# Kernel optimization log

Hardware: AMD Instinct MI355X
Metric: run time of the kernel (lower is better)

The kernel has to match this reference:

```python
import jax, jax.numpy as jnp
import numpy as np

NPOINT = 1024
RADIUS = 0.4
NSAMPLE = 32
BN_EPS = 1e-3  # keras BatchNormalization default epsilon


def _fps(xyz, npoint):
    # xyz: [N,3] -> indices [npoint] via farthest point sampling (seed index 0)
    N = xyz.shape[0]

    def step(carry, _):
        dists, far = carry
        d = jnp.sum((xyz - xyz[far]) ** 2, axis=-1)
        dists = jnp.minimum(dists, d)
        return (dists, jnp.argmax(dists).astype(jnp.int32)), far

    init = (jnp.full((N,), 1e10, dtype=xyz.dtype), jnp.asarray(0, dtype=jnp.int32))
    _, idx = jax.lax.scan(step, init, None, length=npoint)
    return idx


def _ball_query(xyz, new_xyz, radius, nsample):
    # xyz: [N,3], new_xyz: [S,3] -> idx [S,nsample]
    # First up-to-nsample points (in original index order) within radius of each
    # center; slots past the count are filled with the first found index
    # (matching the CUDA query_ball_point semantics).
    N = xyz.shape[0]
    d2 = jnp.sum((new_xyz[:, None, :] - xyz[None, :, :]) ** 2, axis=-1)  # [S,N]
    key = jnp.where(d2 < radius * radius, jnp.arange(N, dtype=jnp.int32), N)
    sk = jnp.sort(key, axis=-1)[:, :nsample]          # first valid indices, padded with N
    first = sk[:, :1]
    first = jnp.where(first < N, first, 0)            # fallback if no neighbor found
    idx = jnp.where(sk < N, sk, first)
    return idx.astype(jnp.int32)


def _gather(pts, idx):
    # pts: [B,N,C], idx: [B,...] -> [B,...,C]
    return jax.vmap(lambda p, i: p[i])(pts, idx)


def _conv_bn_relu(x, W, b, g, be):
    # 1x1 conv over [B,P,S,Cin] + batchnorm (training mode, batch stats) + relu
    y = jnp.einsum('bpsc,co->bpso', x, W) + b
    m = jnp.mean(y, axis=(0, 1, 2))
    v = jnp.var(y, axis=(0, 1, 2))
    y = (y - m) * jax.lax.rsqrt(v + BN_EPS) * g + be
    return jax.nn.relu(y)


def setup_inputs() -> dict:
    key = jax.random.key(0)
    ks = jax.random.split(key, 8)
    B, N, C = 16, 4096, 64
    xyz = jax.random.normal(ks[0], (B, N, 3), dtype=jnp.float32)
    points = jax.random.normal(ks[1], (B, N, C), dtype=jnp.float32)
    chans = [3 + C, 64, 64, 128]
    inp = {'xyz': xyz, 'points': points}
    for i in range(3):
        cin, cout = chans[i], chans[i + 1]
        limit = np.sqrt(6.0 / (cin + cout))  # glorot uniform
        inp[f'W{i}'] = jax.random.uniform(ks[2 + i], (cin, cout), jnp.float32, -limit, limit)
        inp[f'b{i}'] = jnp.zeros((cout,), jnp.float32)
        inp[f'g{i}'] = jnp.ones((cout,), jnp.float32)
        inp[f'be{i}'] = jnp.zeros((cout,), jnp.float32)
    return inp


def reference(xyz, points, W0, b0, g0, be0, W1, b1, g1, be1, W2, b2, g2, be2):
    xyz_c = jax.lax.stop_gradient(xyz)
    fps_idx = jax.vmap(lambda p: _fps(p, NPOINT))(xyz_c)           # [B,NPOINT]
    new_xyz = _gather(xyz, fps_idx)                                 # [B,NPOINT,3]
    idx = jax.vmap(lambda p, c: _ball_query(p, c, RADIUS, NSAMPLE))(
        xyz_c, jax.lax.stop_gradient(new_xyz))                      # [B,NPOINT,NSAMPLE]
    grouped_xyz = _gather(xyz, idx) - new_xyz[:, :, None, :]        # centered local coords
    grouped_points = _gather(points, idx)                           # [B,NPOINT,NSAMPLE,C]
    new_points = jnp.concatenate([grouped_xyz, grouped_points], axis=-1)
    new_points = _conv_bn_relu(new_points, W0, b0, g0, be0)
    new_points = _conv_bn_relu(new_points, W1, b1, g1, be1)
    new_points = _conv_bn_relu(new_points, W2, b2, g2, be2)
    new_points = jnp.max(new_points, axis=2)                        # max-pool over nsample
    return (new_xyz, new_points, idx)
```

## Files before the change

### kernel.cpp

```cpp
#include <hip/hip_runtime.h>

static constexpr int NB      = 16;
static constexpr int NPTS    = 4096;
static constexpr int NPOINTS = 1024;
static constexpr int NSAMP   = 32;
static constexpr int CIN0    = 67;
static constexpr int C0      = 64;
static constexpr int C1      = 64;
static constexpr int C2      = 128;
static constexpr size_t MROWS = (size_t)NB * NPOINTS * NSAMP;
#define RAD2 0.16f
#define BN_EPS 0.001f

__device__ __forceinline__ float4 uld4(const float* __restrict__ p) {
    return *(const float4* __restrict__)p;
}

__device__ __forceinline__ unsigned short f2bf(float f) {
    const unsigned u = __float_as_uint(f);
    return (unsigned short)((u + 0x7fffu + ((u >> 16) & 1u)) >> 16);
}
__device__ __forceinline__ float bf2f(unsigned short h) {
    return __uint_as_float((unsigned)h << 16);
}
// ... 112 lines not shown

    float px[8], py[8], pz[8], dd[8];
#pragma unroll
    for (int j = 0; j < 8; ++j) {
        const int i = tid + j * 512;
        px[j] = sx[i]; py[j] = sy[i]; pz[j] = sz[i];
        dd[j] = 1e10f;
    }

    int   far = 0;
    float fx = sx[0], fy = sy[0], fz = sz[0];
#pragma unroll 1
    for (int it = 0; it < NPOINTS; ++it) {
        if (tid == 0) sidx[it] = far;
        float bv = -1.0f; int bi = 0;
#pragma unroll
        for (int j = 0; j < 8; ++j) {
            const float dx = __fsub_rn(px[j], fx);
            const float dy = __fsub_rn(py[j], fy);
            const float dz = __fsub_rn(pz[j], fz);
            const float d  = __fadd_rn(__fadd_rn(__fmul_rn(dx, dx), __fmul_rn(dy, dy)),
                                       __fmul_rn(dz, dz));
            dd[j] = fminf(dd[j], d);
            if (dd[j] > bv) { bv = dd[j]; bi = tid + j * 512; }
        }
        unsigned long long k = ((unsigned long long)__float_as_uint(bv) << 32)
                             | (unsigned)(4095 - bi);
        kstep<0x111>(k);
        kstep<0x112>(k);
        kstep<0x114>(k);
        kstep<0x118>(k);
        kstep<0x142>(k);
        kstep<0x143>(k);

        const int pb = it & 1;
        if (lane == 63) redk[pb][wv] = k;
        __syncthreads();
        unsigned long long ck = redk[pb][0];
#pragma unroll
        for (int w = 1; w < 8; ++w) {
            const unsigned long long ok = redk[pb][w];
            if (ok > ck) ck = ok;
        }
        const int ci = 4095 - (int)(unsigned)(ck & 0xffffffffull);
        far = ci;
        fx = sx[ci]; fy = sy[ci]; fz = sz[ci];
    }
    __syncthreads();
    for (int it = tid; it < NPOINTS; it += 512) {
        const int ii = sidx[it];
        float* o = out_newxyz + ((size_t)b * NPOINTS + it) * 3;
        o[0] = sx[ii]; o[1] = sy[ii]; o[2] = sz[ii];
    }
}

__global__ __launch_bounds__(256) void ball_kernel(const float* __restrict__ xyz,
                                                   const float* __restrict__ newxyz,
                                                   float* __restrict__ out_idx_f)
{
    __shared__ int sel[4][NSAMP];
    const int tid  = threadIdx.x;
    const int lane = tid & 63;
    const int widx = tid >> 6;
    const int w = blockIdx.x * 4 + widx;
    const int b = w >> 10;

    const float cx = newxyz[(size_t)w * 3 + 0];
    const float cy = newxyz[(size_t)w * 3 + 1];
    const float cz = newxyz[(size_t)w * 3 + 2];
    const float* base = xyz + (size_t)b * NPTS * 3;

    int total = 0;
    for (int c = 0; c < NPTS / 64 && total < NSAMP; ++c) {
        const int n = c * 64 + lane;
        const float dx = __fsub_rn(cx, base[n * 3 + 0]);
        const float dy = __fsub_rn(cy, base[n * 3 + 1]);
        const float dz = __fsub_rn(cz, base[n * 3 + 2]);
        const float d2 = __fadd_rn(__fadd_rn(__fmul_rn(dx, dx), __fmul_rn(dy, dy)),
                                   __fmul_rn(dz, dz));
        const bool pred = d2 < RAD2;
        const unsigned long long mask = __ballot(pred);
        if (pred) {
            const int pos = total + (int)__popcll(mask & ((1ull << lane) - 1ull));
            if (pos < NSAMP) sel[widx][pos] = n;
        }
        total += (int)__popcll(mask);
    }
    __syncthreads();
    if (lane < NSAMP) {
        const int first = sel[widx][0];
        const int v = (lane < total) ? sel[widx][lane] : first;
        out_idx_f[(size_t)w * NSAMP + lane] = (float)v;
    }
}

__device__ __forceinline__ void stats4q(float a0, float a1, float a2, float a3,
                                        float* sa, bool wr)
{
    float q0 = a0*a0, q1 = a1*a1, q2 = a2*a2, q3 = a3*a3;
    a0 = dpp_psum16(a0); q0 = dpp_psum16(q0);
    a1 = dpp_psum16(a1); q1 = dpp_psum16(q1);
    a2 = dpp_psum16(a2); q2 = dpp_psum16(q2);
    a3 = dpp_psum16(a3); q3 = dpp_psum16(q3);
    if (wr) {
        sa[0] += a0; sa[1] += q0; sa[2] += a1; sa[3] += q1;
        sa[4] += a2; sa[5] += q2; sa[6] += a3; sa[7] += q3;
    }
}

__device__ __forceinline__ void stats4(float a0, float a1, float a2, float a3,
                                       float* sa, int lane)
{
    float q0 = a0*a0, q1 = a1*a1, q2 = a2*a2, q3 = a3*a3;
    a0 = dpp_sum64(a0); q0 = dpp_sum64(q0);
    a1 = dpp_sum64(a1); q1 = dpp_sum64(q1);
    a2 = dpp_sum64(a2); q2 = dpp_sum64(q2);
    a3 = dpp_sum64(a3); q3 = dpp_sum64(q3);
    if (lane == 63) {
        sa[0] += a0; sa[1] += q0; sa[2] += a1; sa[3] += q1;
        sa[4] += a2; sa[5] += q2; sa[6] += a3; sa[7] += q3;
    }
}

__device__ __forceinline__ void layer0_dedup(
    const float* __restrict__ xyz, const float* __restrict__ P,
    const float* __restrict__ newxyz, const float* __restrict__ idxf,
    const float* __restrict__ W0, const float* __restrict__ b0,
    int r, float* x1)
{
    const int i  = (int)idxf[r];
    const int bb = r >> 15;
    const int pp = (r >> 5) & 1023;
    const float* pz = xyz + ((size_t)bb * NPTS + i) * 3;
    const float* nz = newxyz + ((size_t)bb * NPOINTS + pp) * 3;
    const float r0 = pz[0] - nz[0];
    const float r1 = pz[1] - nz[1];
    const float r2 = pz[2] - nz[2];
    const float4* prow = (const float4*)(P + ((size_t)bb * NPTS + i) * 64);
#pragma unroll
    for (int oc = 0; oc < 16; ++oc) {
        const float4 pv = prow[oc];
        const float4 bv = uld4(b0 + 4 * oc);
        const float4 wa = uld4(W0 + 0 * 64 + 4 * oc);
        const float4 wb = uld4(W0 + 1 * 64 + 4 * oc);
        const float4 wc = uld4(W0 + 2 * 64 + 4 * oc);
        x1[4*oc+0] = fmaf(r0, wa.x, fmaf(r1, wb.x, fmaf(r2, wc.x, bv.x + pv.x)));
        x1[4*oc+1] = fmaf(r0, wa.y, fmaf(r1, wb.y, fmaf(r2, wc.y, bv.y + pv.y)));
        x1[4*oc+2] = fmaf(r0, wa.z, fmaf(r1, wb.z, fmaf(r2, wc.z, bv.z + pv.z)));
        x1[4*oc+3] = fmaf(r0, wa.w, fmaf(r1, wb.w, fmaf(r2, wc.w, bv.w + pv.w)));
    }
}

__global__ __launch_bounds__(256, 4) void pass0_kernel(
    const float* __restrict__ xyz, const float* __restrict__ P,
    const float* __restrict__ newxyz, const float* __restrict__ idxf,
    const float* __restrict__ W0, const float* __restrict__ b0,
    float* __restrict__ gstats)
{
    __shared__ float sacc[16][2 * C0];
    const int tid  = threadIdx.x;
    const int lane = tid & 63;
    const int wv   = tid >> 6;
    const int slot = wv * 4 + (lane >> 4);
    const bool wr  = (lane & 15) == 15;

    for (int j = tid; j < 16 * 2 * C0; j += 256) (&sacc[0][0])[j] = 0.f;
    __syncthreads();

    const int r = blockIdx.x * 256 + tid;
    float x1[C0];
    layer0_dedup(xyz, P, newxyz, idxf, W0, b0, r, x1);

#pragma unroll
    for (int oc = 0; oc < 16; ++oc)
        stats4q(x1[4*oc+0], x1[4*oc+1], x1[4*oc+2], x1[4*oc+3], &sacc[slot][8*oc], wr);

    __syncthreads();
    for (int j = tid; j < 2 * C0; j += 256) {
        float s = 0.f;
#pragma unroll
        for (int q = 0; q < 16; ++q) s += sacc[q][j];
        atomicAdd(&gstats[j], s);
    }
}

__global__ __launch_bounds__(256, 3) void pass1Y_kernel(
    const float* __restrict__ xyz, const float* __restrict__ P,
    const float* __restrict__ newxyz, const float* __restrict__ idxf,
    const float* __restrict__ W0, const float* __restrict__ b0,
    const float* __restrict__ W1, const float* __restrict__ b1,
    const float* __restrict__ ss0,
    float* __restrict__ gstats, unsigned short* __restrict__ y1b)
{
    __shared__ float sacc[16][2 * C0];
    const int tid  = threadIdx.x;
    const int lane = tid & 63;
    const int wv   = tid >> 6;
    const int slot = wv * 4 + (lane >> 4);
    const bool wr  = (lane & 15) == 15;

    for (int j = tid; j < 16 * 2 * C0; j += 256) (&sacc[0][0])[j] = 0.f;
    __syncthreads();

    const int r = blockIdx.x * 256 + tid;
    float x1[C0];
    layer0_dedup(xyz, P, newxyz, idxf, W0, b0, r, x1);
#pragma unroll
    for (int o = 0; o < C0; ++o)
        x1[o] = fmaxf(0.f, fmaf(x1[o], ss0[o], ss0[64 + o]));

    float y1[C1];
#pragma unroll
    for (int o = 0; o < C1; o += 4) {
        const float4 bv = uld4(b1 + o);
        y1[o] = bv.x; y1[o+1] = bv.y; y1[o+2] = bv.z; y1[o+3] = bv.w;
    }
#pragma unroll 2
    for (int k = 0; k < C0; ++k) {
        const float xk = x1[k];
#pragma unroll
        for (int oc = 0; oc < 16; ++oc) {
            const float4 w4 = uld4(W1 + k * 64 + 4 * oc);
            y1[4*oc+0] = fmaf(xk, w4.x, y1[4*oc+0]);
            y1[4*oc+1] = fmaf(xk, w4.y, y1[4*oc+1]);
            y1[4*oc+2] = fmaf(xk, w4.z, y1[4*oc+2]);
            y1[4*oc+3] = fmaf(xk, w4.w, y1[4*oc+3]);
        }
    }

#pragma unroll
    for (int oc = 0; oc < 16; ++oc)
        stats4q(y1[4*oc+0], y1[4*oc+1], y1[4*oc+2], y1[4*oc+3], &sacc[slot][8*oc], wr);

    uint4* yo = (uint4*)(y1b + (size_t)r * 64);
#pragma unroll
    for (int gq = 0; gq < 8; ++gq) {
        union { unsigned short u[8]; uint4 v; } pk;
#pragma unroll
        for (int e = 0; e < 8; ++e) pk.u[e] = f2bf(y1[8*gq+e]);
        yo[gq] = pk.v;
    }

    __syncthreads();
    for (int j = tid; j < 2 * C0; j += 256) {
        float s = 0.f;
#pragma unroll
        for (int q = 0; q < 16; ++q) s += sacc[q][j];
        atomicAdd(&gstats[j], s);
    }
}

__global__ __launch_bounds__(256, 3) void p2Ym_kernel(
    const unsigned short* __restrict__ y1b,
    const unsigned short* __restrict__ W2t,
    const float* __restrict__ b2,
    const float* __restrict__ ss1,
    float* __restrict__ gstats, float2* __restrict__ mnmx)
{
    __shared__ float  ssl[2 * C1];
    __shared__ float2 sacc[8][C2];
    __shared__ float2 mnacc[8][C2];

    const int tid  = threadIdx.x;
    const int lane = tid & 63;
    const int w    = tid >> 6;
    const int half = lane >> 5;
    const int col  = lane & 31;
    const int slot = w * 2 + half;

    for (int j = tid; j < 2 * C1; j += 256) ssl[j] = ss1[j];
    __syncthreads();

    const int r = blockIdx.x * 128 + w * 32 + col;

    UB afrag[4];
#pragma unroll
    for (int t = 0; t < 4; ++t) {
        const int ko = t * 16 + half * 8;
        uint4 ua = *(const uint4*)(y1b + (size_t)r * 64 + ko);
        float scs[8], shs[8];
        *(float4*)&scs[0] = *(const float4*)&ssl[ko];
        *(float4*)&scs[4] = *(const float4*)&ssl[ko + 4];
        *(float4*)&shs[0] = *(const float4*)&ssl[64 + ko];
        *(float4*)&shs[4] = *(const float4*)&ssl[64 + ko + 4];
        const unsigned* ud = (const unsigned*)&ua;
        uint4 outw;
        unsigned* od = (unsigned*)&outw;
#pragma unroll
        for (int d = 0; d < 4; ++d) {
            const float flo = bf2f((unsigned short)(ud[d] & 0xffffu));
            const float fhi = bf2f((unsigned short)(ud[d] >> 16));
            const float vlo = fmaxf(0.f, fmaf(flo, scs[2*d],   shs[2*d]));
            const float vhi = fmaxf(0.f, fmaf(fhi, scs[2*d+1], shs[2*d+1]));
            od[d] = ((unsigned)f2bf(vhi) << 16) | (unsigned)f2bf(vlo);
        }
        afrag[t].u = outw;
    }

#pragma unroll
    for (int ct = 0; ct < 4; ++ct) {
        const float bias = b2[ct * 32 + col];
        f32x16 acc;
#pragma unroll
        for (int i = 0; i < 16; ++i) acc[i] = bias;
#pragma unroll
        for (int t = 0; t < 4; ++t) {
            UB bfrag;
            bfrag.u = *(const uint4*)(W2t + (size_t)(ct * 32 + col) * 64 + t * 16 + half * 8);
            acc = __builtin_amdgcn_mfma_f32_32x32x16_bf16(afrag[t].h, bfrag.h, acc, 0, 0, 0);
        }
        float s = 0.f, q = 0.f, mn = 3.4e38f, mx = -3.4e38f;
#pragma unroll
        for (int i = 0; i < 16; ++i) {
            const float v = acc[i];
            s += v; q = fmaf(v, v, q);
            mn = fminf(mn, v); mx = fmaxf(mx, v);
        }
        sacc[slot][ct * 32 + col]  = make_float2(s, q);
        mnacc[slot][ct * 32 + col] = make_float2(mn, mx);
    }

    __syncthreads();
    for (int j = tid; j < C2; j += 256) {
        float s = 0.f, q = 0.f;
#pragma unroll
        for (int v = 0; v < 8; ++v) { s += sacc[v][j].x; q += sacc[v][j].y; }
        atomicAdd(&gstats[2*j], s);
        atomicAdd(&gstats[2*j+1], q);
    }
    for (int j = tid; j < 4 * C2; j += 256) {
        const int wg = j >> 7, ch = j & 127;
        const float2 a = mnacc[2*wg][ch], bq = mnacc[2*wg+1][ch];
        mnmx[((size_t)blockIdx.x * 4 + wg) * C2 + ch] =
            make_float2(fminf(a.x, bq.x), fmaxf(a.y, bq.y));
    }
}

__global__ __launch_bounds__(256) void finY_kernel(const float2* __restrict__ mnmx,
                                                   const float* __restrict__ gs2,
                                                   const float* __restrict__ g2,
                                                   const float* __restrict__ be2,
                                                   float* __restrict__ out_np)
{
    const int t = blockIdx.x * 256 + threadIdx.x;
    const int g = t >> 7;
    const int o = t & 127;
    const float inv  = 1.0f / (float)MROWS;
    const float mean = gs2[2*o] * inv;
    const float var  = fmaxf(0.f, gs2[2*o+1] * inv - mean * mean);
    const float sc   = g2[o] / sqrtf(var + BN_EPS);
    const float sh   = fmaf(-mean, sc, be2[o]);
    const float2 mm  = mnmx[(size_t)g * C2 + o];
    const float y    = (sc >= 0.f) ? mm.y : mm.x;
    out_np[t] = fmaxf(0.f, fmaf(y, sc, sh));
}

template<int C>
__global__ void ss_kernel(const float* __restrict__ gs, const float* __restrict__ g,
                          const float* __restrict__ be, float* __restrict__ ss)
{
    const int o = threadIdx.x;
    const float inv  = 1.0f / (float)MROWS;
    const float mean = gs[2*o] * inv;
    const float var  = fmaxf(0.f, gs[2*o+1] * inv - mean * mean);
    const float sc   = g[o] / sqrtf(var + BN_EPS);
    ss[o]     = sc;
    ss[C + o] = fmaf(-mean, sc, be[o]);
}

__global__ __launch_bounds__(256) void preP_kernel(const float* __restrict__ points,
                                                   const float* __restrict__ W0,
                                                   float* __restrict__ P)
{
    const int r = blockIdx.x * 256 + threadIdx.x;
    const float4* pr = (const float4*)(points + (size_t)r * 64);
    float x[64];
#pragma unroll
    for (int j = 0; j < 16; ++j) {
        const float4 v = pr[j];
        x[4*j+0] = v.x; x[4*j+1] = v.y; x[4*j+2] = v.z; x[4*j+3] = v.w;
    }
    float acc[64];
#pragma unroll
    for (int o = 0; o < 64; ++o) acc[o] = 0.f;
#pragma unroll 2
    for (int k = 0; k < 64; ++k) {
        const float xk = x[k];
#pragma unroll
        for (int oc = 0; oc < 16; ++oc) {
            const float4 w4 = uld4(W0 + (3 + k) * 64 + 4 * oc);
            acc[4*oc+0] = fmaf(xk, w4.x, acc[4*oc+0]);
            acc[4*oc+1] = fmaf(xk, w4.y, acc[4*oc+1]);
            acc[4*oc+2] = fmaf(xk, w4.z, acc[4*oc+2]);
            acc[4*oc+3] = fmaf(xk, w4.w, acc[4*oc+3]);
        }
    }
    float4* po = (float4*)(P + (size_t)r * 64);
#pragma unroll
    for (int oc = 0; oc < 16; ++oc)
        po[oc] = make_float4(acc[4*oc+0], acc[4*oc+1], acc[4*oc+2], acc[4*oc+3]);
}

template<int PHASE>
__global__ __launch_bounds__(256, 2) void passP_kernel(
    const float* __restrict__ xyz, const float* __restrict__ P,
    const float* __restrict__ newxyz, const float* __restrict__ idxf,
    const float* __restrict__ W0, const float* __restrict__ b0,
    const float* __restrict__ W1, const float* __restrict__ b1,
    const float* __restrict__ W2, const float* __restrict__ b2,
    const float* __restrict__ ss0, const float* __restrict__ ss1,
    const float* __restrict__ ss2,
    float* __restrict__ gstats, float* __restrict__ out_np)
{
    constexpr int CS = (PHASE == 2) ? C2 : C0;
    __shared__ float sacc[4][2 * CS];

    const int tid  = threadIdx.x;
    const int lane = tid & 63;
    const int wv   = tid >> 6;

    if constexpr (PHASE <= 2) {
        for (int j = tid; j < 8 * CS; j += 256) (&sacc[0][0])[j] = 0.f;
        __syncthreads();
    }

    const int r = blockIdx.x * 256 + tid;
    float x1[C0];
    layer0_dedup(xyz, P, newxyz, idxf, W0, b0, r, x1);

    if constexpr (PHASE == 0) {
#pragma unroll
        for (int oc = 0; oc < 16; ++oc)
            stats4(x1[4*oc+0], x1[4*oc+1], x1[4*oc+2], x1[4*oc+3], &sacc[wv][8*oc], lane);
    } else {
#pragma unroll
        for (int o = 0; o < C0; ++o)
            x1[o] = fmaxf(0.f, fmaf(x1[o], ss0[o], ss0[64 + o]));

        float y1[C1];
#pragma unroll
        for (int o = 0; o < C1; o += 4) {
            const float4 bv = uld4(b1 + o);
            y1[o] = bv.x; y1[o+1] = bv.y; y1[o+2] = bv.z; y1[o+3] = bv.w;
        }
#pragma unroll 2
        for (int k = 0; k < C0; ++k) {
            const float xk = x1[k];
#pragma unroll
            for (int oc = 0; oc < 16; ++oc) {
                const float4 w4 = uld4(W1 + k * 64 + 4 * oc);
                y1[4*oc+0] = fmaf(xk, w4.x, y1[4*oc+0]);
                y1[4*oc+1] = fmaf(xk, w4.y, y1[4*oc+1]);
                y1[4*oc+2] = fmaf(xk, w4.z, y1[4*oc+2]);
// ... 3 lines not shown

        if constexpr (PHASE == 1) {
#pragma unroll
            for (int oc = 0; oc < 16; ++oc)
                stats4(y1[4*oc+0], y1[4*oc+1], y1[4*oc+2], y1[4*oc+3], &sacc[wv][8*oc], lane);
        } else {
#pragma unroll
            for (int o = 0; o < C1; ++o)
                y1[o] = fmaxf(0.f, fmaf(y1[o], ss1[o], ss1[64 + o]));

            float a2[C2];
#pragma unroll
            for (int o = 0; o < C2; o += 4) {
                const float4 bv = uld4(b2 + o);
                a2[o] = bv.x; a2[o+1] = bv.y; a2[o+2] = bv.z; a2[o+3] = bv.w;
            }
#pragma unroll 2
            for (int k = 0; k < C1; ++k) {
                const float xk = y1[k];
#pragma unroll
                for (int o = 0; o < C2; o += 4) {
                    const float4 w4 = uld4(W2 + k * C2 + o);
                    a2[o+0] = fmaf(xk, w4.x, a2[o+0]);
                    a2[o+1] = fmaf(xk, w4.y, a2[o+1]);
                    a2[o+2] = fmaf(xk, w4.z, a2[o+2]);
                    a2[o+3] = fmaf(xk, w4.w, a2[o+3]);
                }
            }

            if constexpr (PHASE == 2) {
#pragma unroll
                for (int o = 0; o < C2; ++o) {
                    const float s = dpp_sum64(a2[o]);
                    const float q = dpp_sum64(a2[o] * a2[o]);
                    if (lane == 63) { sacc[wv][2*o] += s; sacc[wv][2*o+1] += q; }
                }
            } else {
                const int g = r >> 5;
#pragma unroll
                for (int o = 0; o < C2; ++o) {
                    float v = fmaxf(0.f, fmaf(a2[o], ss2[o], ss2[C2 + o]));
                    v = dpp_max32(v);
                    if (lane == 31 || lane == 63) out_np[(size_t)g * C2 + o] = v;
                }
            }
        }
    }

    if constexpr (PHASE <= 2) {
        __syncthreads();
        for (int j = tid; j < 2 * CS; j += 256)
            atomicAdd(&gstats[j], sacc[0][j] + sacc[1][j] + sacc[2][j] + sacc[3][j]);
    }
}

template<int PHASE>
__global__ __launch_bounds__(128) void pass_kernel(
    const float* __restrict__ xyz, const float* __restrict__ points,
    const float* __restrict__ newxyz, const float* __restrict__ idxf,
    const float* __restrict__ W0, const float* __restrict__ b0,
    const float* __restrict__ W1, const float* __restrict__ b1,
    const float* __restrict__ W2, const float* __restrict__ b2,
    const float* __restrict__ ss0, const float* __restrict__ ss1,
    const float* __restrict__ ss2,
    float* __restrict__ gstats, float* __restrict__ out_np)
{
    constexpr int CS = (PHASE == 2) ? C2 : C0;
    __shared__ float xld[(PHASE >= 1) ? (64 * 128) : 1];
    __shared__ float sacc[2][2 * CS];

    const int tid  = threadIdx.x;
    const int lane = tid & 63;
    const int wv   = tid >> 6;

    if constexpr (PHASE <= 2) {
        for (int j = tid; j < 2 * 2 * CS; j += 128) (&sacc[0][0])[j] = 0.f;
        __syncthreads();
    }

    const int r  = blockIdx.x * 128 + tid;
    const int i  = (int)idxf[r];
    const int bb = r >> 15;
    const int pp = (r >> 5) & 1023;

    float x[CIN0];
    {
        const float* pz = xyz + ((size_t)bb * NPTS + i) * 3;
        const float* nz = newxyz + ((size_t)bb * NPOINTS + pp) * 3;
        x[0] = pz[0] - nz[0];
        x[1] = pz[1] - nz[1];
        x[2] = pz[2] - nz[2];
        const float4* p4 = (const float4*)(points + ((size_t)bb * NPTS + i) * 64);
#pragma unroll
        for (int j = 0; j < 16; ++j) {
            const float4 v = p4[j];
            x[3+4*j+0] = v.x; x[3+4*j+1] = v.y; x[3+4*j+2] = v.z; x[3+4*j+3] = v.w;
        }
    }

#pragma unroll 1
    for (int oc = 0; oc < 16; ++oc) {
        const float4 bv = uld4(b0 + 4*oc);
        float a0 = bv.x, a1 = bv.y, a2 = bv.z, a3 = bv.w;
#pragma unroll
        for (int k = 0; k < CIN0; ++k) {
            const float4 w4 = uld4(W0 + k*64 + 4*oc);
// ... 83 lines not shown
        __syncthreads();
        for (int j = tid; j < 2 * CS; j += 128)
            atomicAdd(&gstats[j], sacc[0][j] + sacc[1][j]);
    }
}

extern "C" void kernel_launch(void* const* d_in, const int* in_sizes, int n_in,
                              void* d_out, int out_size, void* d_ws, size_t ws_size,
                              hipStream_t stream)
{
    (void)in_sizes; (void)n_in; (void)out_size;
    const float* xyz    = (const float*)d_in[0];
    const float* points = (const float*)d_in[1];
    const float* W0  = (const float*)d_in[2];
    const float* b0  = (const float*)d_in[3];
    const float* g0  = (const float*)d_in[4];
    const float* be0 = (const float*)d_in[5];
    const float* W1  = (const float*)d_in[6];
    const float* b1  = (const float*)d_in[7];
    const float* g1  = (const float*)d_in[8];
    const float* be1 = (const float*)d_in[9];
    const float* W2  = (const float*)d_in[10];
    const float* b2  = (const float*)d_in[11];
    const float* g2  = (const float*)d_in[12];
    const float* be2 = (const float*)d_in[13];

    float* out = (float*)d_out;
    float* out_newxyz = out;
    float* out_newpts = out + (size_t)NB * NPOINTS * 3;
    float* out_idx    = out_newpts + (size_t)NB * NPOINTS * C2;

    float* wsf = (float*)d_ws;
    float* gs0 = wsf + 0;
    float* gs1 = wsf + 128;
    float* gs2 = wsf + 256;
    float* ss0 = wsf + 512;
    float* ss1 = wsf + 640;
    float* ss2 = wsf + 768;
    const size_t PBYTES  = (size_t)NB * NPTS * C0 * 4;
    const size_t MMBYTES = (size_t)NB * NPOINTS * 2 * C2 * 4;
    const size_t YBYTES  = MROWS * C1 * 2;
    const size_t TBYTES  = (size_t)C2 * C1 * 2;
    float* P    = (float*)((char*)d_ws + 65536);
    float* mnmx = (float*)((char*)d_ws + 65536 + PBYTES);
    unsigned short* y1b = (unsigned short*)((char*)d_ws + 65536 + PBYTES + MMBYTES);
    unsigned short* W2t = (unsigned short*)((char*)d_ws + 65536 + PBYTES + MMBYTES + YBYTES);

    const bool haveP = ws_size >= (65536 + PBYTES);
    const bool haveY = ws_size >= (65536 + PBYTES + MMBYTES + YBYTES + TBYTES);

    const int frontGrid = NB + 1 + (haveP ? (NB * NPTS / 512) : 0);
    fps_kernel<<<frontGrid, 512, 0, stream>>>(xyz, out_newxyz, wsf, points, W0, P,
                                              W2, haveY ? W2t : nullptr);
    ball_kernel<<<(NB * NPOINTS) / 4, 256, 0, stream>>>(xyz, out_newxyz, out_idx);

    if (haveY) {
        const int grid = (int)(MROWS / 256);
        pass0_kernel<<<grid, 256, 0, stream>>>(xyz, P, out_newxyz, out_idx,
                                               W0, b0, gs0);
        ss_kernel<C0><<<1, C0, 0, stream>>>(gs0, g0, be0, ss0);
        pass1Y_kernel<<<grid, 256, 0, stream>>>(xyz, P, out_newxyz, out_idx,
                                                W0, b0, W1, b1, ss0, gs1, y1b);
        ss_kernel<C1><<<1, C1, 0, stream>>>(gs1, g1, be1, ss1);
        p2Ym_kernel<<<(int)(MROWS / 128), 256, 0, stream>>>(y1b, W2t, b2, ss1,
                                                            gs2, (float2*)mnmx);
        finY_kernel<<<NB * NPOINTS * C2 / 256, 256, 0, stream>>>((const float2*)mnmx,
                                                                 gs2, g2, be2, out_newpts);
    } else if (haveP) {
        const int grid = (int)(MROWS / 256);
        passP_kernel<0><<<grid, 256, 0, stream>>>(xyz, P, out_newxyz, out_idx,
                                                  W0, b0, W1, b1, W2, b2,
                                                  ss0, ss1, ss2, gs0, nullptr);
        ss_kernel<C0><<<1, C0, 0, stream>>>(gs0, g0, be0, ss0);
        passP_kernel<1><<<grid, 256, 0, stream>>>(xyz, P, out_newxyz, out_idx,
                                                  W0, b0, W1, b1, W2, b2,
                                                  ss0, ss1, ss2, gs1, nullptr);
        ss_kernel<C1><<<1, C1, 0, stream>>>(gs1, g1, be1, ss1);
        passP_kernel<2><<<grid, 256, 0, stream>>>(xyz, P, out_newxyz, out_idx,
                                                  W0, b0, W1, b1, W2, b2,
                                                  ss0, ss1, ss2, gs2, nullptr);
        ss_kernel<C2><<<1, C2, 0, stream>>>(gs2, g2, be2, ss2);
        passP_kernel<3><<<grid, 256, 0, stream>>>(xyz, P, out_newxyz, out_idx,
                                                  W0, b0, W1, b1, W2, b2,
                                                  ss0, ss1, ss2, nullptr, out_newpts);
    } else {
        const int grid = (int)(MROWS / 128);
        pass_kernel<0><<<grid, 128, 0, stream>>>(xyz, points, out_newxyz, out_idx,
                                                 W0, b0, W1, b1, W2, b2,
                                                 ss0, ss1, ss2, gs0, nullptr);
        ss_kernel<C0><<<1, C0, 0, stream>>>(gs0, g0, be0, ss0);
        pass_kernel<1><<<grid, 128, 0, stream>>>(xyz, points, out_newxyz, out_idx,
                                                 W0, b0, W1, b1, W2, b2,
                                                 ss0, ss1, ss2, gs1, nullptr);
        ss_kernel<C1><<<1, C1, 0, stream>>>(gs1, g1, be1, ss1);
        pass_kernel<2><<<grid, 128, 0, stream>>>(xyz, points, out_newxyz, out_idx,
                                                 W0, b0, W1, b1, W2, b2,
                                                 ss0, ss1, ss2, gs2, nullptr);
        ss_kernel<C2><<<1, C2, 0, stream>>>(gs2, g2, be2, ss2);
        pass_kernel<3><<<grid, 128, 0, stream>>>(xyz, points, out_newxyz, out_idx,
                                                 W0, b0, W1, b1, W2, b2,
                                                 ss0, ss1, ss2, nullptr, out_newpts);
    }
}
```

Measured before the change: 1.202 ms.

## Fuse ball query into layer-0 stats pass and inline BN scale computation

```diff
diff --git a/kernel.cpp b/kernel.cpp
--- a/kernel.cpp
+++ b/kernel.cpp
@@ -188,6 +188,336 @@
         float* o = out_newxyz + ((size_t)b * NPOINTS + it) * 3;
         o[0] = sx[ii]; o[1] = sy[ii]; o[2] = sz[ii];
     }
+}
+
+__device__ __forceinline__ void stats4q(float a0, float a1, float a2, float a3,
+                                        float* sa, bool wr)
+{
+    float q0 = a0*a0, q1 = a1*a1, q2 = a2*a2, q3 = a3*a3;
+    a0 = dpp_psum16(a0); q0 = dpp_psum16(q0);
+    a1 = dpp_psum16(a1); q1 = dpp_psum16(q1);
+    a2 = dpp_psum16(a2); q2 = dpp_psum16(q2);
+    a3 = dpp_psum16(a3); q3 = dpp_psum16(q3);
+    if (wr) {
+        sa[0] += a0; sa[1] += q0; sa[2] += a1; sa[3] += q1;
+        sa[4] += a2; sa[5] += q2; sa[6] += a3; sa[7] += q3;
+    }
+}
+
+__device__ __forceinline__ void stats4(float a0, float a1, float a2, float a3,
+                                       float* sa, int lane)
+{
+    float q0 = a0*a0, q1 = a1*a1, q2 = a2*a2, q3 = a3*a3;
+    a0 = dpp_sum64(a0); q0 = dpp_sum64(q0);
+    a1 = dpp_sum64(a1); q1 = dpp_sum64(q1);
+    a2 = dpp_sum64(a2); q2 = dpp_sum64(q2);
+    a3 = dpp_sum64(a3); q3 = dpp_sum64(q3);
+    if (lane == 63) {
+        sa[0] += a0; sa[1] += q0; sa[2] += a1; sa[3] += q1;
+        sa[4] += a2; sa[5] += q2; sa[6] += a3; sa[7] += q3;
+    }
+}
+
+__device__ __forceinline__ void layer0_body(
+    const float* __restrict__ xyz, const float* __restrict__ P,
+    const float* __restrict__ newxyz,
+    const float* __restrict__ W0, const float* __restrict__ b0,
+    int i, int bb, int pp, float* x1)
+{
+    const float* pz = xyz + ((size_t)bb * NPTS + i) * 3;
+    const float* nz = newxyz + ((size_t)bb * NPOINTS + pp) * 3;
+    const float r0 = pz[0] - nz[0];
+    const float r1 = pz[1] - nz[1];
+    const float r2 = pz[2] - nz[2];
+    const float4* prow = (const float4*)(P + ((size_t)bb * NPTS + i) * 64);
+#pragma unroll
+    for (int oc = 0; oc < 16; ++oc) {
+        const float4 pv = prow[oc];
+        const float4 bv = uld4(b0 + 4 * oc);
+        const float4 wa = uld4(W0 + 0 * 64 + 4 * oc);
+        const float4 wb = uld4(W0 + 1 * 64 + 4 * oc);
+        const float4 wc = uld4(W0 + 2 * 64 + 4 * oc);
+        x1[4*oc+0] = fmaf(r0, wa.x, fmaf(r1, wb.x, fmaf(r2, wc.x, bv.x + pv.x)));
+        x1[4*oc+1] = fmaf(r0, wa.y, fmaf(r1, wb.y, fmaf(r2, wc.y, bv.y + pv.y)));
+        x1[4*oc+2] = fmaf(r0, wa.z, fmaf(r1, wb.z, fmaf(r2, wc.z, bv.z + pv.z)));
+        x1[4*oc+3] = fmaf(r0, wa.w, fmaf(r1, wb.w, fmaf(r2, wc.w, bv.w + pv.w)));
+    }
+}
+
+__device__ __forceinline__ void layer0_dedup(
+    const float* __restrict__ xyz, const float* __restrict__ P,
+    const float* __restrict__ newxyz, const float* __restrict__ idxf,
+    const float* __restrict__ W0, const float* __restrict__ b0,
+    int r, float* x1)
+{
+    const int i  = (int)idxf[r];
+    const int bb = r >> 15;
+    const int pp = (r >> 5) & 1023;
+    layer0_body(xyz, P, newxyz, W0, b0, i, bb, pp, x1);
+}
+
+template<int C>
+__device__ __forceinline__ void bn_inline(const float* __restrict__ gs,
+                                          const float* __restrict__ g,
+                                          const float* __restrict__ be,
+                                          float* ssl, int tid)
+{
+    if (tid < C) {
+        const float inv  = 1.0f / (float)MROWS;
+        const float mean = gs[2*tid] * inv;
+        const float var  = fmaxf(0.f, gs[2*tid+1] * inv - mean * mean);
+        const float sc   = g[tid] / sqrtf(var + BN_EPS);
+        ssl[tid]     = sc;
+        ssl[C + tid] = fmaf(-mean, sc, be[tid]);
+    }
+}
+
+__global__ __launch_bounds__(256, 4) void ballP0_kernel(
+    const float* __restrict__ xyz, const float* __restrict__ P,
+    const float* __restrict__ newxyz,
+    const float* __restrict__ W0, const float* __restrict__ b0,
+    float* __restrict__ gstats, float* __restrict__ out_idx_f)
+{
+    __shared__ int   sel[8][NSAMP];
+    __shared__ int   stotal[8];
+    __shared__ float sacc[16][2 * C0];
+
+    const int tid  = threadIdx.x;
+    const int lane = tid & 63;
+    const int wv   = tid >> 6;
+
+    for (int j = tid; j < 16 * 2 * C0; j += 256) (&sacc[0][0])[j] = 0.f;
+
+#pragma unroll 1
+    for (int cc = 0; cc < 2; ++cc) {
+        const int lc = wv * 2 + cc;
+        const int w  = blockIdx.x * 8 + lc;
+        const int b  = w >> 10;
+        const float cx = newxyz[(size_t)w * 3 + 0];
+        const float cy = newxyz[(size_t)w * 3 + 1];
+        const float cz = newxyz[(size_t)w * 3 + 2];
+        const float* base = xyz + (size_t)b * NPTS * 3;
+
+        int total = 0;
+        for (int c = 0; c < NPTS / 64 && total < NSAMP; ++c) {
+            const int n = c * 64 + lane;
+            const float dx = __fsub_rn(cx, base[n * 3 + 0]);
+            const float dy = __fsub_rn(cy, base[n * 3 + 1]);
+            const float dz = __fsub_rn(cz, base[n * 3 + 2]);
+            const float d2 = __fadd_rn(__fadd_rn(__fmul_rn(dx, dx), __fmul_rn(dy, dy)),
+                                       __fmul_rn(dz, dz));
+            const bool pred = d2 < RAD2;
+            const unsigned long long mask = __ballot(pred);
+            if (pred) {
+                const int pos = total + (int)__popcll(mask & ((1ull << lane) - 1ull));
+                if (pos < NSAMP) sel[lc][pos] = n;
+            }
+            total += (int)__popcll(mask);
+        }
+        if (lane == 0) stotal[lc] = (total < NSAMP) ? total : NSAMP;
+    }
+    __syncthreads();
+
+    const int r  = blockIdx.x * 256 + tid;
+    const int ci = tid >> 5;
+    const int s  = tid & 31;
+    const int tt = stotal[ci];
+    const int n  = (s < tt) ? sel[ci][s] : sel[ci][0];
+    out_idx_f[r] = (float)n;
+
+    const int bb = r >> 15;
+    const int pp = (r >> 5) & 1023;
+    float x1[C0];
+    layer0_body(xyz, P, newxyz, W0, b0, n, bb, pp, x1);
+
+    const int slot = wv * 4 + (lane >> 4);
+    const bool wr  = (lane & 15) == 15;
+#pragma unroll
+    for (int oc = 0; oc < 16; ++oc)
+        stats4q(x1[4*oc+0], x1[4*oc+1], x1[4*oc+2], x1[4*oc+3], &sacc[slot][8*oc], wr);
+
+    __syncthreads();
+    for (int j = tid; j < 2 * C0; j += 256) {
+        float ssum = 0.f;
+#pragma unroll
+        for (int q = 0; q < 16; ++q) ssum += sacc[q][j];
+        atomicAdd(&gstats[j], ssum);
+    }
+}
+
+__global__ __launch_bounds__(256, 3) void pass1Y_kernel(
+    const float* __restrict__ xyz, const float* __restrict__ P,
+    const float* __restrict__ newxyz, const float* __restrict__ idxf,
+    const float* __restrict__ W0, const float* __restrict__ b0,
+    const float* __restrict__ W1, const float* __restrict__ b1,
+    const float* __restrict__ gs0, const float* __restrict__ g0,
+    const float* __restrict__ be0,
+    float* __restrict__ gstats, unsigned short* __restrict__ y1b)
+{
+    __shared__ float sacc[16][2 * C0];
+    __shared__ float ssl[2 * C0];
+    const int tid  = threadIdx.x;
+    const int lane = tid & 63;
+    const int wv   = tid >> 6;
+    const int slot = wv * 4 + (lane >> 4);
+    const bool wr  = (lane & 15) == 15;
+
+    for (int j = tid; j < 16 * 2 * C0; j += 256) (&sacc[0][0])[j] = 0.f;
+    bn_inline<C0>(gs0, g0, be0, ssl, tid);
+    __syncthreads();
+
+    const int r = blockIdx.x * 256 + tid;
+    float x1[C0];
+    layer0_dedup(xyz, P, newxyz, idxf, W0, b0, r, x1);
+#pragma unroll
+    for (int o = 0; o < C0; ++o)
+        x1[o] = fmaxf(0.f, fmaf(x1[o], ssl[o], ssl[64 + o]));
+
+    float y1[C1];
+#pragma unroll
+    for (int o = 0; o < C1; o += 4) {
+        const float4 bv = uld4(b1 + o);
+        y1[o] = bv.x; y1[o+1] = bv.y; y1[o+2] = bv.z; y1[o+3] = bv.w;
+    }
+#pragma unroll 2
+    for (int k = 0; k < C0; ++k) {
+        const float xk = x1[k];
+#pragma unroll
+        for (int oc = 0; oc < 16; ++oc) {
+            const float4 w4 = uld4(W1 + k * 64 + 4 * oc);
+            y1[4*oc+0] = fmaf(xk, w4.x, y1[4*oc+0]);
+            y1[4*oc+1] = fmaf(xk, w4.y, y1[4*oc+1]);
+            y1[4*oc+2] = fmaf(xk, w4.z, y1[4*oc+2]);
+            y1[4*oc+3] = fmaf(xk, w4.w, y1[4*oc+3]);
+        }
+    }
+
+#pragma unroll
+    for (int oc = 0; oc < 16; ++oc)
+        stats4q(y1[4*oc+0], y1[4*oc+1], y1[4*oc+2], y1[4*oc+3], &sacc[slot][8*oc], wr);
+
+    uint4* yo = (uint4*)(y1b + (size_t)r * 64);
+#pragma unroll
+    for (int gq = 0; gq < 8; ++gq) {
+        union { unsigned short u[8]; uint4 v; } pk;
+#pragma unroll
+        for (int e = 0; e < 8; ++e) pk.u[e] = f2bf(y1[8*gq+e]);
+        yo[gq] = pk.v;
+    }
+
+    __syncthreads();
+    for (int j = tid; j < 2 * C0; j += 256) {
+        float s = 0.f;
+#pragma unroll
+        for (int q = 0; q < 16; ++q) s += sacc[q][j];
+        atomicAdd(&gstats[j], s);
+    }
+}
+
+__global__ __launch_bounds__(256, 3) void p2Ym_kernel(
+    const unsigned short* __restrict__ y1b,
+    const unsigned short* __restrict__ W2t,
+    const float* __restrict__ b2,
+    const float* __restrict__ gs1, const float* __restrict__ g1,
+    const float* __restrict__ be1,
+    float* __restrict__ gstats, float2* __restrict__ mnmx)
+{
+    __shared__ float  ssl[2 * C1];
+    __shared__ float2 sacc[8][C2];
+    __shared__ float2 mnacc[8][C2];
+
+    const int tid  = threadIdx.x;
+    const int lane = tid & 63;
+    const int w    = tid >> 6;
+    const int half = lane >> 5;
+    const int col  = lane & 31;
+    const int slot = w * 2 + half;
+
+    bn_inline<C1>(gs1, g1, be1, ssl, tid);
+    __syncthreads();
+
+    const int r = blockIdx.x * 128 + w * 32 + col;
+
+    UB afrag[4];
+#pragma unroll
+    for (int t = 0; t < 4; ++t) {
+        const int ko = t * 16 + half * 8;
+        uint4 ua = *(const uint4*)(y1b + (size_t)r * 64 + ko);
+        float scs[8], shs[8];
+        *(float4*)&scs[0] = *(const float4*)&ssl[ko];
+        *(float4*)&scs[4] = *(const float4*)&ssl[ko + 4];
+        *(float4*)&shs[0] = *(const float4*)&ssl[64 + ko];
+        *(float4*)&shs[4] = *(const float4*)&ssl[64 + ko + 4];
+        const unsigned* ud = (const unsigned*)&ua;
+        uint4 outw;
+        unsigned* od = (unsigned*)&outw;
+#pragma unroll
+        for (int d = 0; d < 4; ++d) {
+            const float flo = bf2f((unsigned short)(ud[d] & 0xffffu));
+            const float fhi = bf2f((unsigned short)(ud[d] >> 16));
+            const float vlo = fmaxf(0.f, fmaf(flo, scs[2*d],   shs[2*d]));
+            const float vhi = fmaxf(0.f, fmaf(fhi, scs[2*d+1], shs[2*d+1]));
+            od[d] = ((unsigned)f2bf(vhi) << 16) | (unsigned)f2bf(vlo);
+        }
+        afrag[t].u = outw;
+    }
+
+#pragma unroll
+    for (int ct = 0; ct < 4; ++ct) {
+        const float bias = b2[ct * 32 + col];
+        f32x16 acc;
+#pragma unroll
+        for (int i = 0; i < 16; ++i) acc[i] = bias;
+#pragma unroll
+        for (int t = 0; t < 4; ++t) {
+            UB bfrag;
+            bfrag.u = *(const uint4*)(W2t + (size_t)(ct * 32 + col) * 64 + t * 16 + half * 8);
+            acc = __builtin_amdgcn_mfma_f32_32x32x16_bf16(afrag[t].h, bfrag.h, acc, 0, 0, 0);
+        }
+        float s = 0.f, q = 0.f, mn = 3.4e38f, mx = -3.4e38f;
+#pragma unroll
+        for (int i = 0; i < 16; ++i) {
+            const float v = acc[i];
+            s += v; q = fmaf(v, v, q);
+            mn = fminf(mn, v); mx = fmaxf(mx, v);
+        }
+        sacc[slot][ct * 32 + col]  = make_float2(s, q);
+        mnacc[slot][ct * 32 + col] = make_float2(mn, mx);
+    }
+
+    __syncthreads();
+    for (int j = tid; j < C2; j += 256) {
+        float s = 0.f, q = 0.f;
+#pragma unroll
+        for (int v = 0; v < 8; ++v) { s += sacc[v][j].x; q += sacc[v][j].y; }
+        atomicAdd(&gstats[2*j], s);
+        atomicAdd(&gstats[2*j+1], q);
+    }
+    for (int j = tid; j < 4 * C2; j += 256) {
+        const int wg = j >> 7, ch = j & 127;
+        const float2 a = mnacc[2*wg][ch], bq = mnacc[2*wg+1][ch];
+        mnmx[((size_t)blockIdx.x * 4 + wg) * C2 + ch] =
+            make_float2(fminf(a.x, bq.x), fmaxf(a.y, bq.y));
+    }
+}
+
+__global__ __launch_bounds__(256) void finY_kernel(const float2* __restrict__ mnmx,
+                                                   const float* __restrict__ gs2,
+                                                   const float* __restrict__ g2,
+                                                   const float* __restrict__ be2,
+                                                   float* __restrict__ out_np)
+{
+    const int t = blockIdx.x * 256 + threadIdx.x;
+    const int g = t >> 7;
+    const int o = t & 127;
+    const float inv  = 1.0f / (float)MROWS;
+    const float mean = gs2[2*o] * inv;
+    const float var  = fmaxf(0.f, gs2[2*o+1] * inv - mean * mean);
+    const float sc   = g2[o] / sqrtf(var + BN_EPS);
+    const float sh   = fmaf(-mean, sc, be2[o]);
+    const float2 mm  = mnmx[(size_t)g * C2 + o];
+    const float y    = (sc >= 0.f) ? mm.y : mm.x;
+    out_np[t] = fmaxf(0.f, fmaf(y, sc, sh));
 }
 
 __global__ __launch_bounds__(256) void ball_kernel(const float* __restrict__ xyz,
@@ -230,267 +560,6 @@
     }
 }
 
-__device__ __forceinline__ void stats4q(float a0, float a1, float a2, float a3,
-                                        float* sa, bool wr)
-{
-    float q0 = a0*a0, q1 = a1*a1, q2 = a2*a2, q3 = a3*a3;
-    a0 = dpp_psum16(a0); q0 = dpp_psum16(q0);
-    a1 = dpp_psum16(a1); q1 = dpp_psum16(q1);
-    a2 = dpp_psum16(a2); q2 = dpp_psum16(q2);
-    a3 = dpp_psum16(a3); q3 = dpp_psum16(q3);
-    if (wr) {
-        sa[0] += a0; sa[1] += q0; sa[2] += a1; sa[3] += q1;
-        sa[4] += a2; sa[5] += q2; sa[6] += a3; sa[7] += q3;
-    }
-}
-
-__device__ __forceinline__ void stats4(float a0, float a1, float a2, float a3,
-                                       float* sa, int lane)
-{
-    float q0 = a0*a0, q1 = a1*a1, q2 = a2*a2, q3 = a3*a3;
-    a0 = dpp_sum64(a0); q0 = dpp_sum64(q0);
-    a1 = dpp_sum64(a1); q1 = dpp_sum64(q1);
-    a2 = dpp_sum64(a2); q2 = dpp_sum64(q2);
-    a3 = dpp_sum64(a3); q3 = dpp_sum64(q3);
-    if (lane == 63) {
-        sa[0] += a0; sa[1] += q0; sa[2] += a1; sa[3] += q1;
-        sa[4] += a2; sa[5] += q2; sa[6] += a3; sa[7] += q3;
-    }
-}
-
-__device__ __forceinline__ void layer0_dedup(
-    const float* __restrict__ xyz, const float* __restrict__ P,
-    const float* __restrict__ newxyz, const float* __restrict__ idxf,
-    const float* __restrict__ W0, const float* __restrict__ b0,
-    int r, float* x1)
-{
-    const int i  = (int)idxf[r];
-    const int bb = r >> 15;
-    const int pp = (r >> 5) & 1023;
-    const float* pz = xyz + ((size_t)bb * NPTS + i) * 3;
-    const float* nz = newxyz + ((size_t)bb * NPOINTS + pp) * 3;
-    const float r0 = pz[0] - nz[0];
-    const float r1 = pz[1] - nz[1];
-    const float r2 = pz[2] - nz[2];
-    const float4* prow = (const float4*)(P + ((size_t)bb * NPTS + i) * 64);
-#pragma unroll
-    for (int oc = 0; oc < 16; ++oc) {
-        const float4 pv = prow[oc];
-        const float4 bv = uld4(b0 + 4 * oc);
-        const float4 wa = uld4(W0 + 0 * 64 + 4 * oc);
-        const float4 wb = uld4(W0 + 1 * 64 + 4 * oc);
-        const float4 wc = uld4(W0 + 2 * 64 + 4 * oc);
-        x1[4*oc+0] = fmaf(r0, wa.x, fmaf(r1, wb.x, fmaf(r2, wc.x, bv.x + pv.x)));
-        x1[4*oc+1] = fmaf(r0, wa.y, fmaf(r1, wb.y, fmaf(r2, wc.y, bv.y + pv.y)));
-        x1[4*oc+2] = fmaf(r0, wa.z, fmaf(r1, wb.z, fmaf(r2, wc.z, bv.z + pv.z)));
-        x1[4*oc+3] = fmaf(r0, wa.w, fmaf(r1, wb.w, fmaf(r2, wc.w, bv.w + pv.w)));
-    }
-}
-
-__global__ __launch_bounds__(256, 4) void pass0_kernel(
-    const float* __restrict__ xyz, const float* __restrict__ P,
-    const float* __restrict__ newxyz, const float* __restrict__ idxf,
-    const float* __restrict__ W0, const float* __restrict__ b0,
-    float* __restrict__ gstats)
-{
-    __shared__ float sacc[16][2 * C0];
-    const int tid  = threadIdx.x;
-    const int lane = tid & 63;
-    const int wv   = tid >> 6;
-    const int slot = wv * 4 + (lane >> 4);
-    const bool wr  = (lane & 15) == 15;
-
-    for (int j = tid; j < 16 * 2 * C0; j += 256) (&sacc[0][0])[j] = 0.f;
-    __syncthreads();
-
-    const int r = blockIdx.x * 256 + tid;
-    float x1[C0];
-    layer0_dedup(xyz, P, newxyz, idxf, W0, b0, r, x1);
-
-#pragma unroll
-    for (int oc = 0; oc < 16; ++oc)
-        stats4q(x1[4*oc+0], x1[4*oc+1], x1[4*oc+2], x1[4*oc+3], &sacc[slot][8*oc], wr);
-
-    __syncthreads();
-    for (int j = tid; j < 2 * C0; j += 256) {
-        float s = 0.f;
-#pragma unroll
-        for (int q = 0; q < 16; ++q) s += sacc[q][j];
-        atomicAdd(&gstats[j], s);
-    }
-}
-
-__global__ __launch_bounds__(256, 3) void pass1Y_kernel(
-    const float* __restrict__ xyz, const float* __restrict__ P,
-    const float* __restrict__ newxyz, const float* __restrict__ idxf,
-    const float* __restrict__ W0, const float* __restrict__ b0,
-    const float* __restrict__ W1, const float* __restrict__ b1,
-    const float* __restrict__ ss0,
-    float* __restrict__ gstats, unsigned short* __restrict__ y1b)
-{
-    __shared__ float sacc[16][2 * C0];
-    const int tid  = threadIdx.x;
-    const int lane = tid & 63;
-    const int wv   = tid >> 6;
-    const int slot = wv * 4 + (lane >> 4);
-    const bool wr  = (lane & 15) == 15;
-
-    for (int j = tid; j < 16 * 2 * C0; j += 256) (&sacc[0][0])[j] = 0.f;
-    __syncthreads();
-
-    const int r = blockIdx.x * 256 + tid;
-    float x1[C0];
-    layer0_dedup(xyz, P, newxyz, idxf, W0, b0, r, x1);
-#pragma unroll
-    for (int o = 0; o < C0; ++o)
-        x1[o] = fmaxf(0.f, fmaf(x1[o], ss0[o], ss0[64 + o]));
-
-    float y1[C1];
-#pragma unroll
-    for (int o = 0; o < C1; o += 4) {
-        const float4 bv = uld4(b1 + o);
-        y1[o] = bv.x; y1[o+1] = bv.y; y1[o+2] = bv.z; y1[o+3] = bv.w;
-    }
-#pragma unroll 2
-    for (int k = 0; k < C0; ++k) {
-        const float xk = x1[k];
-#pragma unroll
-        for (int oc = 0; oc < 16; ++oc) {
-            const float4 w4 = uld4(W1 + k * 64 + 4 * oc);
-            y1[4*oc+0] = fmaf(xk, w4.x, y1[4*oc+0]);
-            y1[4*oc+1] = fmaf(xk, w4.y, y1[4*oc+1]);
-            y1[4*oc+2] = fmaf(xk, w4.z, y1[4*oc+2]);
-            y1[4*oc+3] = fmaf(xk, w4.w, y1[4*oc+3]);
-        }
-    }
-
-#pragma unroll
-    for (int oc = 0; oc < 16; ++oc)
-        stats4q(y1[4*oc+0], y1[4*oc+1], y1[4*oc+2], y1[4*oc+3], &sacc[slot][8*oc], wr);
-
-    uint4* yo = (uint4*)(y1b + (size_t)r * 64);
-#pragma unroll
-    for (int gq = 0; gq < 8; ++gq) {
-        union { unsigned short u[8]; uint4 v; } pk;
-#pragma unroll
-        for (int e = 0; e < 8; ++e) pk.u[e] = f2bf(y1[8*gq+e]);
-        yo[gq] = pk.v;
-    }
-
-    __syncthreads();
-    for (int j = tid; j < 2 * C0; j += 256) {
-        float s = 0.f;
-#pragma unroll
-        for (int q = 0; q < 16; ++q) s += sacc[q][j];
-        atomicAdd(&gstats[j], s);
-    }
-}
-
-__global__ __launch_bounds__(256, 3) void p2Ym_kernel(
-    const unsigned short* __restrict__ y1b,
-    const unsigned short* __restrict__ W2t,
-    const float* __restrict__ b2,
-    const float* __restrict__ ss1,
-    float* __restrict__ gstats, float2* __restrict__ mnmx)
-{
-    __shared__ float  ssl[2 * C1];
-    __shared__ float2 sacc[8][C2];
-    __shared__ float2 mnacc[8][C2];
-
-    const int tid  = threadIdx.x;
-    const int lane = tid & 63;
-    const int w    = tid >> 6;
-    const int half = lane >> 5;
-    const int col  = lane & 31;
-    const int slot = w * 2 + half;
-
-    for (int j = tid; j < 2 * C1; j += 256) ssl[j] = ss1[j];
-    __syncthreads();
-
-    const int r = blockIdx.x * 128 + w * 32 + col;
-
-    UB afrag[4];
-#pragma unroll
-    for (int t = 0; t < 4; ++t) {
-        const int ko = t * 16 + half * 8;
-        uint4 ua = *(const uint4*)(y1b + (size_t)r * 64 + ko);
-        float scs[8], shs[8];
-        *(float4*)&scs[0] = *(const float4*)&ssl[ko];
-        *(float4*)&scs[4] = *(const float4*)&ssl[ko + 4];
-        *(float4*)&shs[0] = *(const float4*)&ssl[64 + ko];
-        *(float4*)&shs[4] = *(const float4*)&ssl[64 + ko + 4];
-        const unsigned* ud = (const unsigned*)&ua;
-        uint4 outw;
-        unsigned* od = (unsigned*)&outw;
-#pragma unroll
-        for (int d = 0; d < 4; ++d) {
-            const float flo = bf2f((unsigned short)(ud[d] & 0xffffu));
-            const float fhi = bf2f((unsigned short)(ud[d] >> 16));
-            const float vlo = fmaxf(0.f, fmaf(flo, scs[2*d],   shs[2*d]));
-            const float vhi = fmaxf(0.f, fmaf(fhi, scs[2*d+1], shs[2*d+1]));
-            od[d] = ((unsigned)f2bf(vhi) << 16) | (unsigned)f2bf(vlo);
-        }
-        afrag[t].u = outw;
-    }
-
-#pragma unroll
-    for (int ct = 0; ct < 4; ++ct) {
-        const float bias = b2[ct * 32 + col];
-        f32x16 acc;
-#pragma unroll
-        for (int i = 0; i < 16; ++i) acc[i] = bias;
-#pragma unroll
-        for (int t = 0; t < 4; ++t) {
-            UB bfrag;
-            bfrag.u = *(const uint4*)(W2t + (size_t)(ct * 32 + col) * 64 + t * 16 + half * 8);
-            acc = __builtin_amdgcn_mfma_f32_32x32x16_bf16(afrag[t].h, bfrag.h, acc, 0, 0, 0);
-        }
-        float s = 0.f, q = 0.f, mn = 3.4e38f, mx = -3.4e38f;
-#pragma unroll
-        for (int i = 0; i < 16; ++i) {
-            const float v = acc[i];
-            s += v; q = fmaf(v, v, q);
-            mn = fminf(mn, v); mx = fmaxf(mx, v);
-        }
-        sacc[slot][ct * 32 + col]  = make_float2(s, q);
-        mnacc[slot][ct * 32 + col] = make_float2(mn, mx);
-    }
-
-    __syncthreads();
-    for (int j = tid; j < C2; j += 256) {
-        float s = 0.f, q = 0.f;
-#pragma unroll
-        for (int v = 0; v < 8; ++v) { s += sacc[v][j].x; q += sacc[v][j].y; }
-        atomicAdd(&gstats[2*j], s);
-        atomicAdd(&gstats[2*j+1], q);
-    }
-    for (int j = tid; j < 4 * C2; j += 256) {
-        const int wg = j >> 7, ch = j & 127;
-        const float2 a = mnacc[2*wg][ch], bq = mnacc[2*wg+1][ch];
-        mnmx[((size_t)blockIdx.x * 4 + wg) * C2 + ch] =
-            make_float2(fminf(a.x, bq.x), fmaxf(a.y, bq.y));
-    }
-}
-
-__global__ __launch_bounds__(256) void finY_kernel(const float2* __restrict__ mnmx,
-                                                   const float* __restrict__ gs2,
-                                                   const float* __restrict__ g2,
-                                                   const float* __restrict__ be2,
-                                                   float* __restrict__ out_np)
-{
-    const int t = blockIdx.x * 256 + threadIdx.x;
-    const int g = t >> 7;
-    const int o = t & 127;
-    const float inv  = 1.0f / (float)MROWS;
-    const float mean = gs2[2*o] * inv;
-    const float var  = fmaxf(0.f, gs2[2*o+1] * inv - mean * mean);
-    const float sc   = g2[o] / sqrtf(var + BN_EPS);
-    const float sh   = fmaf(-mean, sc, be2[o]);
-    const float2 mm  = mnmx[(size_t)g * C2 + o];
-    const float y    = (sc >= 0.f) ? mm.y : mm.x;
-    out_np[t] = fmaxf(0.f, fmaf(y, sc, sh));
-}
-
 template<int C>
 __global__ void ss_kernel(const float* __restrict__ gs, const float* __restrict__ g,
                           const float* __restrict__ be, float* __restrict__ ss)
@@ -502,39 +571,6 @@
     const float sc   = g[o] / sqrtf(var + BN_EPS);
     ss[o]     = sc;
     ss[C + o] = fmaf(-mean, sc, be[o]);
-}
-
-__global__ __launch_bounds__(256) void preP_kernel(const float* __restrict__ points,
-                                                   const float* __restrict__ W0,
-                                                   float* __restrict__ P)
-{
-    const int r = blockIdx.x * 256 + threadIdx.x;
-    const float4* pr = (const float4*)(points + (size_t)r * 64);
-    float x[64];
-#pragma unroll
-    for (int j = 0; j < 16; ++j) {
-        const float4 v = pr[j];
-        x[4*j+0] = v.x; x[4*j+1] = v.y; x[4*j+2] = v.z; x[4*j+3] = v.w;
-    }
-    float acc[64];
-#pragma unroll
-    for (int o = 0; o < 64; ++o) acc[o] = 0.f;
-#pragma unroll 2
-    for (int k = 0; k < 64; ++k) {
-        const float xk = x[k];
-#pragma unroll
-        for (int oc = 0; oc < 16; ++oc) {
-            const float4 w4 = uld4(W0 + (3 + k) * 64 + 4 * oc);
-            acc[4*oc+0] = fmaf(xk, w4.x, acc[4*oc+0]);
-            acc[4*oc+1] = fmaf(xk, w4.y, acc[4*oc+1]);
-            acc[4*oc+2] = fmaf(xk, w4.z, acc[4*oc+2]);
-            acc[4*oc+3] = fmaf(xk, w4.w, acc[4*oc+3]);
-        }
-    }
-    float4* po = (float4*)(P + (size_t)r * 64);
-#pragma unroll
-    for (int oc = 0; oc < 16; ++oc)
-        po[oc] = make_float4(acc[4*oc+0], acc[4*oc+1], acc[4*oc+2], acc[4*oc+3]);
 }
 
 template<int PHASE>
@@ -644,6 +680,39 @@
         for (int j = tid; j < 2 * CS; j += 256)
             atomicAdd(&gstats[j], sacc[0][j] + sacc[1][j] + sacc[2][j] + sacc[3][j]);
     }
+}
+
+__global__ __launch_bounds__(256) void preP_kernel(const float* __restrict__ points,
+                                                   const float* __restrict__ W0,
+                                                   float* __restrict__ P)
+{
+    const int r = blockIdx.x * 256 + threadIdx.x;
+    const float4* pr = (const float4*)(points + (size_t)r * 64);
+    float x[64];
+#pragma unroll
+    for (int j = 0; j < 16; ++j) {
+        const float4 v = pr[j];
+        x[4*j+0] = v.x; x[4*j+1] = v.y; x[4*j+2] = v.z; x[4*j+3] = v.w;
+    }
+    float acc[64];
+#pragma unroll
+    for (int o = 0; o < 64; ++o) acc[o] = 0.f;
+#pragma unroll 2
+    for (int k = 0; k < 64; ++k) {
+        const float xk = x[k];
+#pragma unroll
+        for (int oc = 0; oc < 16; ++oc) {
+            const float4 w4 = uld4(W0 + (3 + k) * 64 + 4 * oc);
+            acc[4*oc+0] = fmaf(xk, w4.x, acc[4*oc+0]);
+            acc[4*oc+1] = fmaf(xk, w4.y, acc[4*oc+1]);
+            acc[4*oc+2] = fmaf(xk, w4.z, acc[4*oc+2]);
+            acc[4*oc+3] = fmaf(xk, w4.w, acc[4*oc+3]);
+        }
+    }
+    float4* po = (float4*)(P + (size_t)r * 64);
+#pragma unroll
+    for (int oc = 0; oc < 16; ++oc)
+        po[oc] = make_float4(acc[4*oc+0], acc[4*oc+1], acc[4*oc+2], acc[4*oc+3]);
 }
 
 template<int PHASE>
@@ -833,22 +902,23 @@
     const int frontGrid = NB + 1 + (haveP ? (NB * NPTS / 512) : 0);
     fps_kernel<<<frontGrid, 512, 0, stream>>>(xyz, out_newxyz, wsf, points, W0, P,
                                               W2, haveY ? W2t : nullptr);
-    ball_kernel<<<(NB * NPOINTS) / 4, 256, 0, stream>>>(xyz, out_newxyz, out_idx);
 
     if (haveY) {
         const int grid = (int)(MROWS / 256);
-        pass0_kernel<<<grid, 256, 0, stream>>>(xyz, P, out_newxyz, out_idx,
-                                               W0, b0, gs0);
-        ss_kernel<C0><<<1, C0, 0, stream>>>(gs0, g0, be0, ss0);
+        ballP0_kernel<<<grid, 256, 0, stream>>>(xyz, P, out_newxyz,
+                                                W0, b0, gs0, out_idx);
         pass1Y_kernel<<<grid, 256, 0, stream>>>(xyz, P, out_newxyz, out_idx,
-                                                W0, b0, W1, b1, ss0, gs1, y1b);
-        ss_kernel<C1><<<1, C1, 0, stream>>>(gs1, g1, be1, ss1);
-        p2Ym_kernel<<<(int)(MROWS / 128), 256, 0, stream>>>(y1b, W2t, b2, ss1,
+                                                W0, b0, W1, b1,
+                                                gs0, g0, be0, gs1, y1b);
+        p2Ym_kernel<<<(int)(MROWS / 128), 256, 0, stream>>>(y1b, W2t, b2,
+                                                            gs1, g1, be1,
                                                             gs2, (float2*)mnmx);
         finY_kernel<<<NB * NPOINTS * C2 / 256, 256, 0, stream>>>((const float2*)mnmx,
                                                                  gs2, g2, be2, out_newpts);
     } else if (haveP) {
+        ball_kernel<<<(NB * NPOINTS) / 4, 256, 0, stream>>>(xyz, out_newxyz, out_idx);
         const int grid = (int)(MROWS / 256);
+        preP_kernel<<<NB * NPTS / 256, 256, 0, stream>>>(points, W0, P);
         passP_kernel<0><<<grid, 256, 0, stream>>>(xyz, P, out_newxyz, out_idx,
                                                   W0, b0, W1, b1, W2, b2,
                                                   ss0, ss1, ss2, gs0, nullptr);
@@ -865,6 +935,7 @@
                                                   W0, b0, W1, b1, W2, b2,
                                                   ss0, ss1, ss2, nullptr, out_newpts);
     } else {
+        ball_kernel<<<(NB * NPOINTS) / 4, 256, 0, stream>>>(xyz, out_newxyz, out_idx);
         const int grid = (int)(MROWS / 128);
         pass_kernel<0><<<grid, 128, 0, stream>>>(xyz, points, out_newxyz, out_idx,
                                                  W0, b0, W1, b1, W2, b2,
```

Result: no change. 1.197 ms (-0.4%).
